# Kernel optimization log

Measured on AMD Instinct MI355X. Metric: run time of the kernel, lower is better.

The kernel has to match this reference:

```python
import jax, jax.numpy as jnp
import numpy as np

C_IN = 128
C_QK = C_IN // 8


def setup_inputs() -> dict:
    key = jax.random.key(0)
    kx, kq, kk, kv = jax.random.split(key, 4)
    x = jax.random.normal(kx, (8, C_IN, 64, 64), dtype=jnp.float32)
    # 1x1 conv weights, stored as (c_out, c_in); fan-in scaled init
    s = 1.0 / np.sqrt(C_IN)
    Wq = jax.random.normal(kq, (C_QK, C_IN), dtype=jnp.float32) * s
    Wk = jax.random.normal(kk, (C_QK, C_IN), dtype=jnp.float32) * s
    Wv = jax.random.normal(kv, (C_IN, C_IN), dtype=jnp.float32) * s
    gamma = jnp.ones((1,), dtype=jnp.float32) * 0.5  # nonzero so residual branch matters
    return {"x": x, "Wq": Wq, "Wk": Wk, "Wv": Wv, "gamma": gamma}


def reference(x, Wq, Wk, Wv, gamma):
    b, c, h, w = x.shape
    xt = rearr = x.reshape(b, c, h * w)            # b c n
    q = jnp.einsum('oc,bcn->bno', Wq, xt)          # b n c//8
    k = jnp.einsum('oc,bcn->bon', Wk, xt)          # b c//8 n
    v = jnp.einsum('oc,bcn->bno', Wv, xt)          # b n c
    energy = jnp.einsum('bno,bom->bnm', q, k)      # b n n (no scale, per source)
    attn = jax.nn.softmax(energy, axis=-1)
    out = jnp.einsum('bnm,bmc->bnc', attn, v)      # b n c
    out = out.transpose(0, 2, 1).reshape(b, c, h, w)
    return x + gamma[0] * out
```

## Files before the change

kernel.cpp:

```cpp
#include <hip/hip_runtime.h>
#include <hip/hip_bf16.h>


typedef __bf16 bf16x8 __attribute__((ext_vector_type(8)));
typedef __bf16 bf16x4 __attribute__((ext_vector_type(4)));
typedef float  f32x16 __attribute__((ext_vector_type(16)));
typedef unsigned int uint32x2 __attribute__((ext_vector_type(2)));

static constexpr int Bb = 8, Cc = 128, Nn = 4096, CQ = 16;

__device__ __forceinline__ f32x16 mfma32(bf16x8 a, bf16x8 b, f32x16 c) {
    return __builtin_amdgcn_mfma_f32_32x32x16_bf16(a, b, c, 0, 0, 0);
}
struct HL { __bf16 h, l; };
__device__ __forceinline__ HL hilo(float f) {
    HL r;
    r.h = (__bf16)f;
    r.l = (__bf16)(f - (float)r.h);
    return r;
}
__device__ __forceinline__ unsigned int pack2bf(float a, float b) {
    union { __bf16 h[2]; unsigned int u; } x;
    x.h[0] = (__bf16)a; x.h[1] = (__bf16)b;
    return x.u;
}

__global__ __launch_bounds__(256, 4) void qkv_kernel(
    const float* __restrict__ x, const float* __restrict__ Wq,
    const float* __restrict__ Wk, const float* __restrict__ Wv,
    __bf16* __restrict__ qw, __bf16* __restrict__ kw, __bf16* __restrict__ vw)
{
    const int b = blockIdx.y, tile = blockIdx.x, n0 = tile * 32, t = threadIdx.x;
    const int wave = t >> 6, lane = t & 63, lr = lane & 31, lq = lane >> 5;

    __shared__ __bf16 xh[32][136], xl[32][136];
    __shared__ __bf16 sc[3][32][40];

    {
        const int n = t & 31, ci0 = (t >> 5) * 16;
        float v[16];
        #pragma unroll
        for (int k = 0; k < 16; ++k)
            v[k] = x[((size_t)(b * Cc + ci0 + k)) * Nn + n0 + n];
        bf16x8 h8[2], l8[2];
        #pragma unroll
        for (int k = 0; k < 16; ++k) {
            HL z = hilo(v[k]);
            h8[k >> 3][k & 7] = z.h;
            l8[k >> 3][k & 7] = z.l;
        }
        *(bf16x8*)&xh[n][ci0]     = h8[0];
        *(bf16x8*)&xh[n][ci0 + 8] = h8[1];
        *(bf16x8*)&xl[n][ci0]     = l8[0];
        *(bf16x8*)&xl[n][ci0 + 8] = l8[1];
    }
    __syncthreads();

    if (wave == 0) {
        const float* wrow = (lr < 16) ? (Wq + (size_t)lr * Cc)
                                      : (Wk + (size_t)(lr - 16) * Cc);
        f32x16 acc = {};
        #pragma unroll
        for (int ks = 0; ks < 8; ++ks) {
            float4 w0 = *(const float4*)(wrow + ks * 16 + lq * 8);
            float4 w1 = *(const float4*)(wrow + ks * 16 + lq * 8 + 4);
            bf16x8 ah, al;
            HL z;
            z = hilo(w0.x); ah[0] = z.h; al[0] = z.l;
            z = hilo(w0.y); ah[1] = z.h; al[1] = z.l;
            z = hilo(w0.z); ah[2] = z.h; al[2] = z.l;
            z = hilo(w0.w); ah[3] = z.h; al[3] = z.l;
            z = hilo(w1.x); ah[4] = z.h; al[4] = z.l;
            z = hilo(w1.y); ah[5] = z.h; al[5] = z.l;
            z = hilo(w1.z); ah[6] = z.h; al[6] = z.l;
            z = hilo(w1.w); ah[7] = z.h; al[7] = z.l;
            bf16x8 bh = *(const bf16x8*)&xh[lr][ks * 16 + lq * 8];
            bf16x8 bl = *(const bf16x8*)&xl[lr][ks * 16 + lq * 8];
            acc = mfma32(ah, bh, acc);
            acc = mfma32(al, bh, acc);
            acc = mfma32(ah, bl, acc);
        }
        __bf16* qb = qw + (((size_t)b * 128 + tile) << 10);
        __bf16* kb = kw + (((size_t)b * 128 + tile) << 10);
        #pragma unroll
        for (int rg = 0; rg < 4; ++rg) {
            bf16x4 h4, l4;
            #pragma unroll
            for (int j = 0; j < 4; ++j) {
                float v = acc[rg * 4 + j];
                if (rg < 2) v *= 1.44269504089f;
                HL z = hilo(v);
                h4[j] = z.h; l4[j] = z.l;
            }
            const int off = (rg & 1) * 256 + lr * 8 + 4 * lq;
            __bf16* base = (rg < 2) ? qb : kb;
            *(bf16x4*)(base + off) = h4;
            *(bf16x4*)(base + 512 + off) = l4;
        }
    } else {
        int cts[2]; int nt;
        if      (wave == 1) { cts[0] = 0; cts[1] = 1; nt = 2; }
        else if (wave == 2) { cts[0] = 2; nt = 1; }
        else                { cts[0] = 3; nt = 1; }
        for (int ti = 0; ti < nt; ++ti) {
            const int ct = cts[ti];
            f32x16 acc = {};
            #pragma unroll
            for (int ks = 0; ks < 8; ++ks) {
                const float* wp = Wv + (size_t)(ct * 32 + lr) * Cc + ks * 16 + lq * 8;
                float4 w0 = *(const float4*)wp;
                float4 w1 = *(const float4*)(wp + 4);
                bf16x8 a = { (__bf16)w0.x, (__bf16)w0.y, (__bf16)w0.z, (__bf16)w0.w,
                             (__bf16)w1.x, (__bf16)w1.y, (__bf16)w1.z, (__bf16)w1.w };
                bf16x8 bh = *(const bf16x8*)&xh[lr][ks * 16 + lq * 8];
                acc = mfma32(a, bh, acc);
            }
            #pragma unroll
            for (int r = 0; r < 16; ++r) {
                int crow = (r & 3) + 8 * (r >> 2) + 4 * lq;
                sc[wave - 1][crow][lr] = (__bf16)acc[r];
            }
            __bf16* vb = vw + (((size_t)b * 128 + tile) << 12) + ct * 1024;
            #pragma unroll
            for (int u = 0; u < 2; ++u) {
                bf16x8 row = *(const bf16x8*)&sc[wave - 1][lr][u * 16 + lq * 8];
                *(bf16x8*)(vb + u * 512 + lane * 8) = row;
            }
        }
    }
}

__global__ __launch_bounds__(512, 4) void attn_kernel(
    const float* __restrict__ x, const __bf16* __restrict__ qw,
    const __bf16* __restrict__ kw, const __bf16* __restrict__ vw,
    const float* __restrict__ gamma, float* __restrict__ out)
{
    const int h = blockIdx.x;
    const int b = h & 7;
    const int qt = h >> 3;
    const int t = threadIdx.x;
    const int wave = t >> 6, lane = t & 63, lr = lane & 31, lq = lane >> 5;
    const int kr = wave & 3, ch = wave >> 2;

    __shared__ float accbuf[32][129];
    __shared__ float lbuf[32];

    const __bf16* qb = qw + (((size_t)b * 128 + qt) << 10) + lane * 8;
    const bf16x8 qhi = *(const bf16x8*)qb;
    const bf16x8 qlo = *(const bf16x8*)(qb + 512);

    const int c0 = kr * 32;
    const __bf16* kp = kw + (((size_t)b * 128 + c0) << 10) + lane * 8;
    const __bf16* vp = vw + (((size_t)b * 128 + c0) << 12) + ch * 2048 + lane * 8;

    f32x16 acc0 = {}, acc1 = {};
    float l_part = 0.f;

    bf16x8 kh = *(const bf16x8*)kp,          kl = *(const bf16x8*)(kp + 512);
    bf16x8 v0 = *(const bf16x8*)vp,          v1 = *(const bf16x8*)(vp + 512);
    bf16x8 v2 = *(const bf16x8*)(vp + 1024), v3 = *(const bf16x8*)(vp + 1536);

    auto body = [&](bf16x8 Kh, bf16x8 Kl, bf16x8 V0, bf16x8 V1,
                    bf16x8 V2, bf16x8 V3) {
        f32x16 s = {};
        s = mfma32(Kh, qhi, s);
        s = mfma32(Kl, qhi, s);
        s = mfma32(Kh, qlo, s);

        float p[16];
        #pragma unroll
        for (int r = 0; r < 16; ++r) p[r] = __builtin_amdgcn_exp2f(s[r]);
        l_part += ((((p[0] + p[1]) + (p[2] + p[3])) + ((p[4] + p[5]) + (p[6] + p[7])))
                 + (((p[8] + p[9]) + (p[10] + p[11])) + ((p[12] + p[13]) + (p[14] + p[15]))));

        unsigned int G00 = pack2bf(p[0],  p[1]),  G01 = pack2bf(p[2],  p[3]);
        unsigned int G10 = pack2bf(p[4],  p[5]),  G11 = pack2bf(p[6],  p[7]);
        unsigned int G20 = pack2bf(p[8],  p[9]),  G21 = pack2bf(p[10], p[11]);
        unsigned int G30 = pack2bf(p[12], p[13]), G31 = pack2bf(p[14], p[15]);

        {
            uint32x2 r;
            r = __builtin_amdgcn_permlane32_swap(G00, G10, false, false);
            G00 = r[0]; G10 = r[1];
            r = __builtin_amdgcn_permlane32_swap(G01, G11, false, false);
            G01 = r[0]; G11 = r[1];
            r = __builtin_amdgcn_permlane32_swap(G20, G30, false, false);
            G20 = r[0]; G30 = r[1];
            r = __builtin_amdgcn_permlane32_swap(G21, G31, false, false);
            G21 = r[0]; G31 = r[1];
        }

        union U8 { unsigned int u[4]; bf16x8 v; };
        U8 F0, F1;
        F0.u[0] = G00; F0.u[1] = G01; F0.u[2] = G10; F0.u[3] = G11;
        F1.u[0] = G20; F1.u[1] = G21; F1.u[2] = G30; F1.u[3] = G31;

        acc0 = mfma32(V0, F0.v, acc0);
        acc0 = mfma32(V1, F1.v, acc0);
        acc1 = mfma32(V2, F0.v, acc1);
        acc1 = mfma32(V3, F1.v, acc1);
    };

    for (int it = 0; it < 31; ++it) {
        kp += 1024; vp += 4096;
        bf16x8 nkh = *(const bf16x8*)kp,          nkl = *(const bf16x8*)(kp + 512);
        bf16x8 nv0 = *(const bf16x8*)vp,          nv1 = *(const bf16x8*)(vp + 512);
        bf16x8 nv2 = *(const bf16x8*)(vp + 1024), nv3 = *(const bf16x8*)(vp + 1536);
        body(kh, kl, v0, v1, v2, v3);
        kh = nkh; kl = nkl; v0 = nv0; v1 = nv1; v2 = nv2; v3 = nv3;
    }
    body(kh, kl, v0, v1, v2, v3);

    l_part += __shfl_xor(l_part, 32);

    if (kr == 0) {
        #pragma unroll
        for (int r = 0; r < 16; ++r) {
            int c = ch * 64 + (r & 3) + 8 * (r >> 2) + 4 * lq;
            accbuf[lr][c] = acc0[r];
            accbuf[lr][c + 32] = acc1[r];
        }
        if (wave == 0 && lane < 32) lbuf[lr] = l_part;
    }
    __syncthreads();
    if (kr != 0) {
        #pragma unroll
        for (int r = 0; r < 16; ++r) {
            int c = ch * 64 + (r & 3) + 8 * (r >> 2) + 4 * lq;
            atomicAdd(&accbuf[lr][c], acc0[r]);
            atomicAdd(&accbuf[lr][c + 32], acc1[r]);
        }
        if (ch == 0 && lane < 32) atomicAdd(&lbuf[lr], l_part);
    }
    __syncthreads();

    const float g = gamma[0];
    const int q = t & 31, cg = t >> 5;
    const float linv = 1.0f / lbuf[q];
    const int n0b = qt * 32;
    #pragma unroll
    for (int i = 0; i < 8; ++i) {
        int c = cg + 16 * i;
        size_t idx = ((size_t)(b * Cc + c)) * Nn + n0b + q;
        out[idx] = x[idx] + g * accbuf[q][c] * linv;
    }
}

extern "C" void kernel_launch(void* const* d_in, const int* in_sizes, int n_in,
                              void* d_out, int out_size, void* d_ws, size_t ws_size,
                              hipStream_t stream) {
    const float* x  = (const float*)d_in[0];
    const float* Wq = (const float*)d_in[1];
    const float* Wk = (const float*)d_in[2];
    const float* Wv = (const float*)d_in[3];
    const float* gm = (const float*)d_in[4];

    __bf16* qw = (__bf16*)d_ws;
    __bf16* kw = qw + (size_t)Bb * 128 * 1024;
    __bf16* vw = kw + (size_t)Bb * 128 * 1024;

    qkv_kernel<<<dim3(Nn / 32, Bb), 256, 0, stream>>>(x, Wq, Wk, Wv, qw, kw, vw);
    attn_kernel<<<dim3(Nn / 32 * Bb), 512, 0, stream>>>(x, qw, kw, vw, gm,
                                                        (float*)d_out);
}
```

Baseline: 191.3 us.

## Pre-permute V rows so softmax P feeds MFMA without permlane swaps

The QKV kernel now writes V with a lane permutation on the key index (klr), so the attention kernel can pack P straight from its accumulator registers into MFMA B operands. This removes the pack2bf and permlane32_swap shuffle from the inner loop. The QKV kernel also grows to 320 threads, giving each V tile its own wave and a separate wave for Q/K, which evens out per-wave work. The attention loop is manually unrolled by two with ping-pong register buffers to keep the prefetch overlapped, at the cost of more register pressure.

```diff
diff --git a/kernel.cpp b/kernel.cpp
--- a/kernel.cpp
+++ b/kernel.cpp
@@ -5,7 +5,6 @@
 typedef __bf16 bf16x8 __attribute__((ext_vector_type(8)));
 typedef __bf16 bf16x4 __attribute__((ext_vector_type(4)));
 typedef float  f32x16 __attribute__((ext_vector_type(16)));
-typedef unsigned int uint32x2 __attribute__((ext_vector_type(2)));
 
 static constexpr int Bb = 8, Cc = 128, Nn = 4096, CQ = 16;
 
@@ -19,13 +18,8 @@
     r.l = (__bf16)(f - (float)r.h);
     return r;
 }
-__device__ __forceinline__ unsigned int pack2bf(float a, float b) {
-    union { __bf16 h[2]; unsigned int u; } x;
-    x.h[0] = (__bf16)a; x.h[1] = (__bf16)b;
-    return x.u;
-}
-
-__global__ __launch_bounds__(256, 4) void qkv_kernel(
+
+__global__ __launch_bounds__(320) void qkv_kernel(
     const float* __restrict__ x, const float* __restrict__ Wq,
     const float* __restrict__ Wk, const float* __restrict__ Wv,
     __bf16* __restrict__ qw, __bf16* __restrict__ kw, __bf16* __restrict__ vw)
@@ -34,9 +28,9 @@
     const int wave = t >> 6, lane = t & 63, lr = lane & 31, lq = lane >> 5;
 
     __shared__ __bf16 xh[32][136], xl[32][136];
-    __shared__ __bf16 sc[3][32][40];
-
-    {
+    __shared__ __bf16 sc[4][32][40];
+
+    if (t < 256) {
         const int n = t & 31, ci0 = (t >> 5) * 16;
         float v[16];
         #pragma unroll
@@ -56,7 +50,7 @@
     }
     __syncthreads();
 
-    if (wave == 0) {
+    if (wave == 4) {
         const float* wrow = (lr < 16) ? (Wq + (size_t)lr * Cc)
                                       : (Wk + (size_t)(lr - 16) * Cc);
         f32x16 acc = {};
@@ -98,34 +92,29 @@
             *(bf16x4*)(base + 512 + off) = l4;
         }
     } else {
-        int cts[2]; int nt;
-        if      (wave == 1) { cts[0] = 0; cts[1] = 1; nt = 2; }
-        else if (wave == 2) { cts[0] = 2; nt = 1; }
-        else                { cts[0] = 3; nt = 1; }
-        for (int ti = 0; ti < nt; ++ti) {
-            const int ct = cts[ti];
-            f32x16 acc = {};
-            #pragma unroll
-            for (int ks = 0; ks < 8; ++ks) {
-                const float* wp = Wv + (size_t)(ct * 32 + lr) * Cc + ks * 16 + lq * 8;
-                float4 w0 = *(const float4*)wp;
-                float4 w1 = *(const float4*)(wp + 4);
-                bf16x8 a = { (__bf16)w0.x, (__bf16)w0.y, (__bf16)w0.z, (__bf16)w0.w,
-                             (__bf16)w1.x, (__bf16)w1.y, (__bf16)w1.z, (__bf16)w1.w };
-                bf16x8 bh = *(const bf16x8*)&xh[lr][ks * 16 + lq * 8];
-                acc = mfma32(a, bh, acc);
-            }
-            #pragma unroll
-            for (int r = 0; r < 16; ++r) {
-                int crow = (r & 3) + 8 * (r >> 2) + 4 * lq;
-                sc[wave - 1][crow][lr] = (__bf16)acc[r];
-            }
-            __bf16* vb = vw + (((size_t)b * 128 + tile) << 12) + ct * 1024;
-            #pragma unroll
-            for (int u = 0; u < 2; ++u) {
-                bf16x8 row = *(const bf16x8*)&sc[wave - 1][lr][u * 16 + lq * 8];
-                *(bf16x8*)(vb + u * 512 + lane * 8) = row;
-            }
+        const int ct = wave;
+        f32x16 acc = {};
+        #pragma unroll
+        for (int ks = 0; ks < 8; ++ks) {
+            const float* wp = Wv + (size_t)(ct * 32 + lr) * Cc + ks * 16 + lq * 8;
+            float4 w0 = *(const float4*)wp;
+            float4 w1 = *(const float4*)(wp + 4);
+            bf16x8 a = { (__bf16)w0.x, (__bf16)w0.y, (__bf16)w0.z, (__bf16)w0.w,
+                         (__bf16)w1.x, (__bf16)w1.y, (__bf16)w1.z, (__bf16)w1.w };
+            bf16x8 bh = *(const bf16x8*)&xh[lr][ks * 16 + lq * 8];
+            acc = mfma32(a, bh, acc);
+        }
+        const int klr = (lr & ~12) | ((lr & 4) << 1) | ((lr & 8) >> 1);
+        #pragma unroll
+        for (int r = 0; r < 16; ++r) {
+            int crow = (r & 3) + 8 * (r >> 2) + 4 * lq;
+            sc[wave][crow][klr] = (__bf16)acc[r];
+        }
+        __bf16* vb = vw + (((size_t)b * 128 + tile) << 12) + ct * 1024;
+        #pragma unroll
+        for (int u = 0; u < 2; ++u) {
+            bf16x8 row = *(const bf16x8*)&sc[wave][lr][u * 16 + lq * 8];
+            *(bf16x8*)(vb + u * 512 + lane * 8) = row;
         }
     }
 }
@@ -156,12 +145,13 @@
     f32x16 acc0 = {}, acc1 = {};
     float l_part = 0.f;
 
-    bf16x8 kh = *(const bf16x8*)kp,          kl = *(const bf16x8*)(kp + 512);
-    bf16x8 v0 = *(const bf16x8*)vp,          v1 = *(const bf16x8*)(vp + 512);
-    bf16x8 v2 = *(const bf16x8*)(vp + 1024), v3 = *(const bf16x8*)(vp + 1536);
-
-    auto body = [&](bf16x8 Kh, bf16x8 Kl, bf16x8 V0, bf16x8 V1,
-                    bf16x8 V2, bf16x8 V3) {
+    bf16x8 akh = *(const bf16x8*)kp,          akl = *(const bf16x8*)(kp + 512);
+    bf16x8 av0 = *(const bf16x8*)vp,          av1 = *(const bf16x8*)(vp + 512);
+    bf16x8 av2 = *(const bf16x8*)(vp + 1024), av3 = *(const bf16x8*)(vp + 1536);
+    bf16x8 bkh, bkl, bv0, bv1, bv2, bv3;
+
+    auto body = [&](const bf16x8& Kh, const bf16x8& Kl, const bf16x8& V0,
+                    const bf16x8& V1, const bf16x8& V2, const bf16x8& V3) {
         f32x16 s = {};
         s = mfma32(Kh, qhi, s);
         s = mfma32(Kl, qhi, s);
@@ -173,43 +163,37 @@
         l_part += ((((p[0] + p[1]) + (p[2] + p[3])) + ((p[4] + p[5]) + (p[6] + p[7])))
                  + (((p[8] + p[9]) + (p[10] + p[11])) + ((p[12] + p[13]) + (p[14] + p[15]))));
 
-        unsigned int G00 = pack2bf(p[0],  p[1]),  G01 = pack2bf(p[2],  p[3]);
-        unsigned int G10 = pack2bf(p[4],  p[5]),  G11 = pack2bf(p[6],  p[7]);
-        unsigned int G20 = pack2bf(p[8],  p[9]),  G21 = pack2bf(p[10], p[11]);
-        unsigned int G30 = pack2bf(p[12], p[13]), G31 = pack2bf(p[14], p[15]);
-
-        {
-            uint32x2 r;
-            r = __builtin_amdgcn_permlane32_swap(G00, G10, false, false);
-            G00 = r[0]; G10 = r[1];
-            r = __builtin_amdgcn_permlane32_swap(G01, G11, false, false);
-            G01 = r[0]; G11 = r[1];
-            r = __builtin_amdgcn_permlane32_swap(G20, G30, false, false);
-            G20 = r[0]; G30 = r[1];
-            r = __builtin_amdgcn_permlane32_swap(G21, G31, false, false);
-            G21 = r[0]; G31 = r[1];
-        }
-
-        union U8 { unsigned int u[4]; bf16x8 v; };
-        U8 F0, F1;
-        F0.u[0] = G00; F0.u[1] = G01; F0.u[2] = G10; F0.u[3] = G11;
-        F1.u[0] = G20; F1.u[1] = G21; F1.u[2] = G30; F1.u[3] = G31;
-
-        acc0 = mfma32(V0, F0.v, acc0);
-        acc0 = mfma32(V1, F1.v, acc0);
-        acc1 = mfma32(V2, F0.v, acc1);
-        acc1 = mfma32(V3, F1.v, acc1);
+        bf16x8 F0, F1;
+        #pragma unroll
+        for (int j = 0; j < 8; ++j) {
+            F0[j] = (__bf16)p[j];
+            F1[j] = (__bf16)p[8 + j];
+        }
+
+        acc0 = mfma32(V0, F0, acc0);
+        acc0 = mfma32(V1, F1, acc0);
+        acc1 = mfma32(V2, F0, acc1);
+        acc1 = mfma32(V3, F1, acc1);
     };
 
-    for (int it = 0; it < 31; ++it) {
+    for (int it = 0; it < 15; ++it) {
         kp += 1024; vp += 4096;
-        bf16x8 nkh = *(const bf16x8*)kp,          nkl = *(const bf16x8*)(kp + 512);
-        bf16x8 nv0 = *(const bf16x8*)vp,          nv1 = *(const bf16x8*)(vp + 512);
-        bf16x8 nv2 = *(const bf16x8*)(vp + 1024), nv3 = *(const bf16x8*)(vp + 1536);
-        body(kh, kl, v0, v1, v2, v3);
-        kh = nkh; kl = nkl; v0 = nv0; v1 = nv1; v2 = nv2; v3 = nv3;
-    }
-    body(kh, kl, v0, v1, v2, v3);
+        bkh = *(const bf16x8*)kp;          bkl = *(const bf16x8*)(kp + 512);
+        bv0 = *(const bf16x8*)vp;          bv1 = *(const bf16x8*)(vp + 512);
+        bv2 = *(const bf16x8*)(vp + 1024); bv3 = *(const bf16x8*)(vp + 1536);
+        body(akh, akl, av0, av1, av2, av3);
+        kp += 1024; vp += 4096;
+        akh = *(const bf16x8*)kp;          akl = *(const bf16x8*)(kp + 512);
+        av0 = *(const bf16x8*)vp;          av1 = *(const bf16x8*)(vp + 512);
+        av2 = *(const bf16x8*)(vp + 1024); av3 = *(const bf16x8*)(vp + 1536);
+        body(bkh, bkl, bv0, bv1, bv2, bv3);
+    }
+    kp += 1024; vp += 4096;
+    bkh = *(const bf16x8*)kp;          bkl = *(const bf16x8*)(kp + 512);
+    bv0 = *(const bf16x8*)vp;          bv1 = *(const bf16x8*)(vp + 512);
+    bv2 = *(const bf16x8*)(vp + 1024); bv3 = *(const bf16x8*)(vp + 1536);
+    body(akh, akl, av0, av1, av2, av3);
+    body(bkh, bkl, bv0, bv1, bv2, bv3);
 
     l_part += __shfl_xor(l_part, 32);
 
@@ -259,7 +243,7 @@
     __bf16* kw = qw + (size_t)Bb * 128 * 1024;
     __bf16* vw = kw + (size_t)Bb * 128 * 1024;
 
-    qkv_kernel<<<dim3(Nn / 32, Bb), 256, 0, stream>>>(x, Wq, Wk, Wv, qw, kw, vw);
+    qkv_kernel<<<dim3(Nn / 32, Bb), 320, 0, stream>>>(x, Wq, Wk, Wv, qw, kw, vw);
     attn_kernel<<<dim3(Nn / 32 * Bb), 512, 0, stream>>>(x, qw, kw, vw, gm,
                                                         (float*)d_out);
 }
```

New measurement: 187.9 us. About the same (-1.8%).
